# Kernel optimization log

Measured on AMD Instinct MI355X. Metric: run time of the kernel, lower is better.

## Reference

```python
import jax, jax.numpy as jnp
import numpy as np
from jax import lax

PATCH = 16  # patch_size


def setup_inputs() -> dict:
    key = jax.random.key(0)
    k1, k2, k3, k4, k5 = jax.random.split(key, 5)
    B, C, H, W = 64, 3, 384, 384
    N, E, P = 576, 768, PATCH
    x = jax.random.normal(k1, (B, C, H, W), dtype=jnp.float32)
    # start = center - patch//2; valid starts are in [0, H-P]
    start_h = jax.random.randint(k2, (B, N), 0, H - P, dtype=jnp.int32)
    start_w = jax.random.randint(k3, (B, N), 0, W - P, dtype=jnp.int32)
    proj_w = jax.random.normal(k4, (E, C, P, P), dtype=jnp.float32) * 0.02
    proj_b = jax.random.normal(k5, (E,), dtype=jnp.float32) * 0.02
    return {"x": x, "start_h": start_h, "start_w": start_w,
            "proj_w": proj_w, "proj_b": proj_b}


def _extract_patch(img, sh, sw):
    # img: [C, H, W] -> [C, P, P]
    return lax.dynamic_slice(img, (0, sh, sw), (img.shape[0], PATCH, PATCH))


def reference(x, start_h, start_w, proj_w, proj_b):
    # Gather patches: vmap over patches, then over batch -> [B, N, C, P, P]
    per_image = jax.vmap(_extract_patch, in_axes=(None, 0, 0))
    patches = jax.vmap(per_image)(x, start_h, start_w)
    # Conv2d with kernel=stride=P on a PxP patch == linear projection + bias
    out = jnp.einsum('bnchw,echw->bne', patches, proj_w) + proj_b
    return out  # [B, N, E]
```

## Files before the change

### kernel.cpp

```cpp
#include <hip/hip_runtime.h>

typedef __attribute__((ext_vector_type(8))) short short8;
typedef __attribute__((ext_vector_type(4))) float f32x4;
typedef unsigned int u32;

#define NB 64
#define NC 3
#define NH 384
#define NW 384
#define HW (NH*NW)
#define NPATCH 576
#define NE 768
#define KDIM 768
#define MDIM (NB*NPATCH)

#define BM 128
#define BN 256
#define BK 64
#define NBLK_N (NE / BN)
#define NBLK_M (MDIM / BM)
#define NWG (NBLK_M * NBLK_N)
#define NKK (KDIM / BK)

#define TILE_B_BYTES (BN * BK * 2)
#define WS_B_BYTES (NBLK_N * NKK * TILE_B_BYTES)

#define GLOBAL_AS __attribute__((address_space(1)))
#define LDS_AS    __attribute__((address_space(3)))

__device__ __forceinline__ unsigned short f2bf(float f) {
    unsigned int u = __builtin_bit_cast(unsigned int, f);
    u += 0x7fffu + ((u >> 16) & 1u);
    return (unsigned short)(u >> 16);
}

__device__ __forceinline__ u32 cvtpk(float lo, float hi) {
    u32 r;
    asm("v_cvt_pk_bf16_f32 %0, %1, %2" : "=v"(r) : "v"(lo), "v"(hi));
    return r;
}

__device__ __forceinline__ void gload_lds16(const void* g, void* l) {
    __builtin_amdgcn_global_load_lds((const GLOBAL_AS u32*)g, (LDS_AS u32*)l, 16, 0, 0);
}

__global__ __launch_bounds__(256) void convert_w(
    const float* __restrict__ pw, unsigned char* __restrict__ wsb)
{
    int id = blockIdx.x * 256 + threadIdx.x;
    int e  = id / 96;
    int ck = id - e * 96;
    int k0 = ck * 8;

    const float4 f0 = *reinterpret_cast<const float4*>(pw + (size_t)e * KDIM + k0);
    const float4 f1 = *reinterpret_cast<const float4*>(pw + (size_t)e * KDIM + k0 + 4);
    u32 a = (u32)f2bf(f0.x) | ((u32)f2bf(f0.y) << 16);
    u32 b = (u32)f2bf(f0.z) | ((u32)f2bf(f0.w) << 16);
    u32 c = (u32)f2bf(f1.x) | ((u32)f2bf(f1.y) << 16);
    u32 d = (u32)f2bf(f1.z) | ((u32)f2bf(f1.w) << 16);

    int bn = e >> 8;
    int r  = e & 255;
    int kk = k0 >> 6;
    int ch = (k0 & 63) >> 3;
    int off = (bn * NKK + kk) * TILE_B_BYTES + r * 128 + ((ch ^ (r & 7)) * 16);
    *reinterpret_cast<uint4*>(wsb + off) = make_uint4(a, b, c, d);
}

template <bool WSB>
__global__ __launch_bounds__(512, 4) void patch_embed_gemm(
    const float* __restrict__ x,
    const int* __restrict__ start_h,
    const int* __restrict__ start_w,
    const float* __restrict__ pw,
    const float* __restrict__ pb,
    const unsigned char* __restrict__ wsb,
    float* __restrict__ out)
{
    __shared__ __align__(16) unsigned short lA[2][BM * BK];
    __shared__ __align__(16) unsigned short lB[BN * BK];
    __shared__ int baseOff[BM];

    const int tid = threadIdx.x;
    const int bid  = blockIdx.x;
    const int lbid = (bid & 7) * (NWG / 8) + (bid >> 3);
    const int bm = lbid / NBLK_N;
    const int bn = lbid - bm * NBLK_N;
    const int m0 = bm * BM;
    const int e0 = bn * BN;

    if (tid < BM) {
        int m = m0 + tid;
        int b = m / NPATCH;
        int n = m - b * NPATCH;
        baseOff[tid] = b * (NC * HW) + start_h[b * NPATCH + n] * NW
                     + start_w[b * NPATCH + n];
    }

    const int lane = tid & 63;
    const int wv   = tid >> 6;
    const int wr   = wv >> 2;
    const int wc   = wv & 3;
    const int lr   = lane & 15;
    const int lk   = lane >> 4;

    const int rt = tid >> 4;
    const int j0 = (tid & 15) * 4;
    const int chunk  = j0 >> 3;
    const int within = j0 & 7;
    const int hsub   = j0 >> 4;
    const int wsub   = j0 & 15;

    __syncthreads();

    int ab[4];
    #pragma unroll
    for (int i = 0; i < 4; ++i)
        ab[i] = baseOff[i * 32 + rt] + hsub * NW + wsub;

    f32x4 acc[4][4] = {};
    float4 ar[4];

#define LOADA(KK)                                                             \
    {                                                                         \
        const int koff = ((KK) >> 2) * HW + ((KK) & 3) * 4 * NW;              \
        _Pragma("unroll")                                                     \
        for (int i = 0; i < 4; ++i)                                           \
            ar[i] = *reinterpret_cast<const float4*>(x + ab[i] + koff);       \
    }

#define WRITEA(BUF)                                                           \
    {                                                                         \
        _Pragma("unroll")                                                     \
        for (int i = 0; i < 4; ++i) {                                         \
            int r = i * 32 + rt;                                              \
            int off = r * BK + ((chunk ^ (r & 7)) * 8) + within;              \
            *reinterpret_cast<uint2*>(&lA[BUF][off]) =                        \
                make_uint2(cvtpk(ar[i].x, ar[i].y), cvtpk(ar[i].z, ar[i].w)); \
        }                                                                     \
    }

#define STAGEB(KK)                                                            \
    if (WSB) {                                                                \
        const unsigned char* src = wsb + (size_t)(bn * NKK + (KK)) * TILE_B_BYTES \
                                 + wv * 1024 + lane * 16;                     \
        unsigned char* dst = reinterpret_cast<unsigned char*>(lB) + wv * 1024;\
        _Pragma("unroll")                                                     \
        for (int i = 0; i < 4; ++i)                                           \
            gload_lds16(src + i * 8192, dst + i * 8192);                      \
    } else {                                                                  \
        _Pragma("unroll")                                                     \
        for (int i = 0; i < 8; ++i) {                                         \
            int r = i * 32 + rt;                                              \
            const float4 wf = *reinterpret_cast<const float4*>(               \
                pw + (size_t)(e0 + r) * KDIM + (KK) * BK + j0);               \
            int off = r * BK + ((chunk ^ (r & 7)) * 8) + within;              \
            *reinterpret_cast<uint2*>(&lB[off]) =                            \
                make_uint2(cvtpk(wf.x, wf.y), cvtpk(wf.z, wf.w));             \
        }                                                                     \
    }

#define COMPUTE(BUF)                                                          \
    {                                                                         \
        _Pragma("unroll")                                                     \
        for (int ks = 0; ks < 2; ++ks) {                                      \
            short8 af[4], bfr[4];                                             \
            _Pragma("unroll")                                                 \
            for (int mi = 0; mi < 4; ++mi) {                                  \
                int row = wr * 64 + mi * 16 + lr;                             \
                int off = row * BK + (((ks * 4 + lk) ^ (row & 7)) * 8);       \
                af[mi] = *reinterpret_cast<const short8*>(&lA[BUF][off]);     \
            }                                                                 \
            _Pragma("unroll")                                                 \
            for (int ni = 0; ni < 4; ++ni) {                                  \
                int row = wc * 64 + ni * 16 + lr;                             \
                int off = row * BK + (((ks * 4 + lk) ^ (row & 7)) * 8);       \
                bfr[ni] = *reinterpret_cast<const short8*>(&lB[off]);         \
            }                                                                 \
            _Pragma("unroll")                                                 \
            for (int mi = 0; mi < 4; ++mi)                                    \
                _Pragma("unroll")                                             \
                for (int ni = 0; ni < 4; ++ni)                                \
                    acc[mi][ni] = __builtin_amdgcn_mfma_f32_16x16x32_bf16(    \
                        af[mi], bfr[ni], acc[mi][ni], 0, 0, 0);               \
        }                                                                     \
    }

    LOADA(0)
    WRITEA(0)
    STAGEB(0)
    __syncthreads();

    for (int kk = 0; kk < NKK; ++kk) {
        const int buf = kk & 1;
        if (kk + 1 < NKK) LOADA(kk + 1)
        COMPUTE(buf)
        __syncthreads();
        if (kk + 1 < NKK) {
            WRITEA(buf ^ 1)
            STAGEB(kk + 1)
        }
        __syncthreads();
    }

#undef LOADA
#undef WRITEA
#undef STAGEB
#undef COMPUTE

    float biasv[4];
    #pragma unroll
    for (int ni = 0; ni < 4; ++ni)
        biasv[ni] = pb[e0 + wc * 64 + ni * 16 + lr];

    #pragma unroll
    for (int mi = 0; mi < 4; ++mi) {
        #pragma unroll
        for (int j = 0; j < 4; ++j) {
            int row = m0 + wr * 64 + mi * 16 + lk * 4 + j;
            float* orow = out + (size_t)row * NE + e0 + wc * 64 + lr;
            #pragma unroll
            for (int ni = 0; ni < 4; ++ni)
                orow[ni * 16] = acc[mi][ni][j] + biasv[ni];
        }
    }
}

extern "C" void kernel_launch(void* const* d_in, const int* in_sizes, int n_in,
                              void* d_out, int out_size, void* d_ws, size_t ws_size,
                              hipStream_t stream) {
    const float* x  = (const float*)d_in[0];
    const int* sh   = (const int*)d_in[1];
    const int* sw   = (const int*)d_in[2];
    const float* pw = (const float*)d_in[3];
    const float* pb = (const float*)d_in[4];
    float* out = (float*)d_out;

    if (ws_size >= (size_t)WS_B_BYTES) {
        unsigned char* wsb = (unsigned char*)d_ws;
        hipLaunchKernelGGL(convert_w, dim3(288), dim3(256), 0, stream, pw, wsb);
        hipLaunchKernelGGL(patch_embed_gemm<true>, dim3(NWG), dim3(512), 0, stream,
                           x, sh, sw, pw, pb, wsb, out);
    } else {
        hipLaunchKernelGGL(patch_embed_gemm<false>, dim3(NWG), dim3(512), 0, stream,
                           x, sh, sw, pw, pb, (const unsigned char*)nullptr, out);
    }
}
```

Measured before the change: 78.35 us.

## Split patch gather into pre-pass and stream pre-packed bf16 tiles into GEMM

Adds a gather kernel that extracts patches from x, converts them to bf16 and writes them into swizzled A tiles in workspace. Adds a weight conversion that writes B in MFMA fragment order, so the new GEMM loads B straight into registers and stages A via direct global-to-LDS loads with double buffering. This removes the irregular gather and fp32-to-bf16 conversion from the GEMM inner loop and frees the B LDS buffer. The cost is an extra kernel launch plus writing and re-reading roughly 57 MB of bf16 A through global memory, and the path depends on the workspace being large enough.

```diff
diff --git a/kernel.cpp b/kernel.cpp
--- a/kernel.cpp
+++ b/kernel.cpp
@@ -22,8 +22,10 @@
 #define NWG (NBLK_M * NBLK_N)
 #define NKK (KDIM / BK)
 
+#define TILE_A_BYTES (BM * BK * 2)
 #define TILE_B_BYTES (BN * BK * 2)
-#define WS_B_BYTES (NBLK_N * NKK * TILE_B_BYTES)
+#define WS_A_BYTES ((size_t)NBLK_M * NKK * TILE_A_BYTES)
+#define WS_B_BYTES ((size_t)NBLK_N * NKK * TILE_B_BYTES)
 
 #define GLOBAL_AS __attribute__((address_space(1)))
 #define LDS_AS    __attribute__((address_space(3)))
@@ -44,7 +46,186 @@
     __builtin_amdgcn_global_load_lds((const GLOBAL_AS u32*)g, (LDS_AS u32*)l, 16, 0, 0);
 }
 
-__global__ __launch_bounds__(256) void convert_w(
+__global__ __launch_bounds__(256) void gather_a(
+    const float* __restrict__ x,
+    const int* __restrict__ start_h,
+    const int* __restrict__ start_w,
+    unsigned char* __restrict__ wsa)
+{
+    int id = blockIdx.x * 256 + threadIdx.x;
+    int m  = id / 96;
+    int ck = id - m * 96;
+    int b  = m / NPATCH;
+    int n  = m - b * NPATCH;
+    int base = b * (NC * HW) + start_h[b * NPATCH + n] * NW
+             + start_w[b * NPATCH + n];
+
+    int gk = ck * 8;
+    int c  = gk >> 8;
+    int h  = (gk & 255) >> 4;
+    int w  = gk & 15;
+    const float* src = x + base + c * HW + h * NW + w;
+    float4 f0 = *reinterpret_cast<const float4*>(src);
+    float4 f1 = *reinterpret_cast<const float4*>(src + 4);
+
+    int bm = m >> 7, r = m & 127, kk = ck >> 3, ch = ck & 7;
+    size_t off = (size_t)(bm * NKK + kk) * TILE_A_BYTES
+               + r * 128 + ((ch ^ (r & 7)) * 16);
+    *reinterpret_cast<uint4*>(wsa + off) = make_uint4(
+        cvtpk(f0.x, f0.y), cvtpk(f0.z, f0.w),
+        cvtpk(f1.x, f1.y), cvtpk(f1.z, f1.w));
+}
+
+__global__ __launch_bounds__(256) void convert_w_frag(
+    const float* __restrict__ pw, unsigned char* __restrict__ wsb)
+{
+    int id = blockIdx.x * 256 + threadIdx.x;
+    int tile = id >> 11;
+    int s    = id & 2047;
+    int bn = tile / NKK;
+    int kk = tile - bn * NKK;
+    int f = s >> 6, l = s & 63;
+    int e = bn * 256 + (f >> 1) * 16 + (l & 15);
+    int k = kk * 64 + (f & 1) * 32 + (l >> 4) * 8;
+
+    const float4 f0 = *reinterpret_cast<const float4*>(pw + (size_t)e * KDIM + k);
+    const float4 f1 = *reinterpret_cast<const float4*>(pw + (size_t)e * KDIM + k + 4);
+    *reinterpret_cast<uint4*>(wsb + (size_t)tile * TILE_B_BYTES + s * 16) =
+        make_uint4(cvtpk(f0.x, f0.y), cvtpk(f0.z, f0.w),
+                   cvtpk(f1.x, f1.y), cvtpk(f1.z, f1.w));
+}
+
+__global__ __launch_bounds__(512, 4) void gemm2(
+    const unsigned char* __restrict__ wsa,
+    const unsigned char* __restrict__ wsb,
+    const float* __restrict__ pb,
+    float* __restrict__ out)
+{
+    __shared__ __align__(16) unsigned short lA[2][BM * BK];
+
+    const int tid = threadIdx.x;
+    const int bid  = blockIdx.x;
+    const int lbid = (bid & 7) * (NWG / 8) + (bid >> 3);
+    const int bm = lbid / NBLK_N;
+    const int bn = lbid - bm * NBLK_N;
+    const int m0 = bm * BM;
+    const int e0 = bn * BN;
+
+    const int lane = tid & 63;
+    const int wv   = tid >> 6;
+    const int wr   = wv >> 2;
+    const int wc   = wv & 3;
+    const int lr   = lane & 15;
+    const int lk   = lane >> 4;
+
+    const unsigned char* atiles = wsa + (size_t)bm * NKK * TILE_A_BYTES;
+    const unsigned char* btiles = wsb + (size_t)bn * NKK * TILE_B_BYTES;
+    unsigned char* lab = reinterpret_cast<unsigned char*>(&lA[0][0]);
+
+    int ard[4];
+    #pragma unroll
+    for (int mi = 0; mi < 4; ++mi) {
+        int row = wr * 64 + mi * 16 + lr;
+        ard[mi] = row * 128;
+    }
+    const int arow7[4] = { (wr*64+0*16+lr) & 7, (wr*64+1*16+lr) & 7,
+                           (wr*64+2*16+lr) & 7, (wr*64+3*16+lr) & 7 };
+
+    uint4 br[8];
+    f32x4 acc[4][4] = {};
+
+#define STAGEA(KK, BUF)                                                       \
+    {                                                                         \
+        const unsigned char* s_ = atiles + (size_t)(KK) * TILE_A_BYTES        \
+                                + wv * 2048 + lane * 16;                      \
+        unsigned char* d_ = lab + (BUF) * 16384 + wv * 2048;                  \
+        gload_lds16(s_, d_);                                                  \
+        gload_lds16(s_ + 1024, d_ + 1024);                                    \
+    }
+
+#define LOADB(KK)                                                             \
+    {                                                                         \
+        const unsigned char* bt = btiles + (size_t)(KK) * TILE_B_BYTES        \
+                                + lane * 16;                                  \
+        _Pragma("unroll")                                                     \
+        for (int f = 0; f < 8; ++f)                                           \
+            br[(f & 1) * 4 + (f >> 1)] = *reinterpret_cast<const uint4*>(     \
+                bt + ((wc * 4 + (f >> 1)) * 2 + (f & 1)) * 1024);             \
+    }
+
+#define COMPUTE(BUF)                                                          \
+    {                                                                         \
+        _Pragma("unroll")                                                     \
+        for (int ks = 0; ks < 2; ++ks) {                                      \
+            short8 af[4];                                                     \
+            _Pragma("unroll")                                                 \
+            for (int mi = 0; mi < 4; ++mi)                                    \
+                af[mi] = *reinterpret_cast<const short8*>(                    \
+                    lab + (BUF) * 16384 + ard[mi]                             \
+                        + (((ks * 4 + lk) ^ arow7[mi]) * 16));                \
+            _Pragma("unroll")                                                 \
+            for (int mi = 0; mi < 4; ++mi)                                    \
+                _Pragma("unroll")                                             \
+                for (int ni = 0; ni < 4; ++ni)                                \
+                    acc[mi][ni] = __builtin_amdgcn_mfma_f32_16x16x32_bf16(    \
+                        af[mi], __builtin_bit_cast(short8, br[ks * 4 + ni]),  \
+                        acc[mi][ni], 0, 0, 0);                                \
+        }                                                                     \
+    }
+
+    STAGEA(0, 0)
+    STAGEA(1, 1)
+    LOADB(0)
+    __builtin_amdgcn_sched_barrier(0);
+    asm volatile("s_waitcnt vmcnt(8)" ::: "memory");
+    __builtin_amdgcn_sched_barrier(0);
+    __builtin_amdgcn_s_barrier();
+
+    #pragma unroll
+    for (int kk = 0; kk < NKK; ++kk) {
+        const int buf = kk & 1;
+        COMPUTE(buf)
+        if (kk + 1 < NKK) LOADB(kk + 1)
+        if (kk + 1 < NKK) {
+            __builtin_amdgcn_sched_barrier(0);
+            __builtin_amdgcn_s_barrier();
+            __builtin_amdgcn_sched_barrier(0);
+            if (kk + 2 < NKK) STAGEA(kk + 2, buf)
+            __builtin_amdgcn_sched_barrier(0);
+            if (kk + 2 < NKK) {
+                asm volatile("s_waitcnt vmcnt(10)" ::: "memory");
+            } else {
+                asm volatile("s_waitcnt vmcnt(8)" ::: "memory");
+            }
+            __builtin_amdgcn_sched_barrier(0);
+            __builtin_amdgcn_s_barrier();
+            __builtin_amdgcn_sched_barrier(0);
+        }
+    }
+
+#undef STAGEA
+#undef LOADB
+#undef COMPUTE
+
+    float biasv[4];
+    #pragma unroll
+    for (int ni = 0; ni < 4; ++ni)
+        biasv[ni] = pb[e0 + wc * 64 + ni * 16 + lr];
+
+    #pragma unroll
+    for (int mi = 0; mi < 4; ++mi) {
+        #pragma unroll
+        for (int j = 0; j < 4; ++j) {
+            int row = m0 + wr * 64 + mi * 16 + lk * 4 + j;
+            float* orow = out + (size_t)row * NE + e0 + wc * 64 + lr;
+            #pragma unroll
+            for (int ni = 0; ni < 4; ++ni)
+                orow[ni * 16] = acc[mi][ni][j] + biasv[ni];
+        }
+    }
+}
+
+__global__ __launch_bounds__(256) void convert_w_row(
     const float* __restrict__ pw, unsigned char* __restrict__ wsb)
 {
     int id = blockIdx.x * 256 + threadIdx.x;
@@ -54,21 +235,19 @@
 
     const float4 f0 = *reinterpret_cast<const float4*>(pw + (size_t)e * KDIM + k0);
     const float4 f1 = *reinterpret_cast<const float4*>(pw + (size_t)e * KDIM + k0 + 4);
-    u32 a = (u32)f2bf(f0.x) | ((u32)f2bf(f0.y) << 16);
-    u32 b = (u32)f2bf(f0.z) | ((u32)f2bf(f0.w) << 16);
-    u32 c = (u32)f2bf(f1.x) | ((u32)f2bf(f1.y) << 16);
-    u32 d = (u32)f2bf(f1.z) | ((u32)f2bf(f1.w) << 16);
-
     int bn = e >> 8;
     int r  = e & 255;
     int kk = k0 >> 6;
     int ch = (k0 & 63) >> 3;
-    int off = (bn * NKK + kk) * TILE_B_BYTES + r * 128 + ((ch ^ (r & 7)) * 16);
-    *reinterpret_cast<uint4*>(wsb + off) = make_uint4(a, b, c, d);
+    size_t off = (size_t)(bn * NKK + kk) * TILE_B_BYTES + r * 128
+               + ((ch ^ (r & 7)) * 16);
+    *reinterpret_cast<uint4*>(wsb + off) = make_uint4(
+        cvtpk(f0.x, f0.y), cvtpk(f0.z, f0.w),
+        cvtpk(f1.x, f1.y), cvtpk(f1.z, f1.w));
 }
 
 template <bool WSB>
-__global__ __launch_bounds__(512, 4) void patch_embed_gemm(
+__global__ __launch_bounds__(512, 4) void fused_gemm(
     const float* __restrict__ x,
     const int* __restrict__ start_h,
     const int* __restrict__ start_w,
@@ -236,13 +415,21 @@
     const float* pb = (const float*)d_in[4];
     float* out = (float*)d_out;
 
-    if (ws_size >= (size_t)WS_B_BYTES) {
+    if (ws_size >= WS_A_BYTES + WS_B_BYTES) {
+        unsigned char* wsa = (unsigned char*)d_ws;
+        unsigned char* wsb = wsa + WS_A_BYTES;
+        hipLaunchKernelGGL(gather_a, dim3(MDIM * 96 / 256), dim3(256), 0, stream,
+                           x, sh, sw, wsa);
+        hipLaunchKernelGGL(convert_w_frag, dim3(288), dim3(256), 0, stream, pw, wsb);
+        hipLaunchKernelGGL(gemm2, dim3(NWG), dim3(512), 0, stream,
+                           wsa, wsb, pb, out);
+    } else if (ws_size >= WS_B_BYTES) {
         unsigned char* wsb = (unsigned char*)d_ws;
-        hipLaunchKernelGGL(convert_w, dim3(288), dim3(256), 0, stream, pw, wsb);
-        hipLaunchKernelGGL(patch_embed_gemm<true>, dim3(NWG), dim3(512), 0, stream,
+        hipLaunchKernelGGL(convert_w_row, dim3(288), dim3(256), 0, stream, pw, wsb);
+        hipLaunchKernelGGL(fused_gemm<true>, dim3(NWG), dim3(512), 0, stream,
                            x, sh, sw, pw, pb, wsb, out);
     } else {
-        hipLaunchKernelGGL(patch_embed_gemm<false>, dim3(NWG), dim3(512), 0, stream,
+        hipLaunchKernelGGL(fused_gemm<false>, dim3(NWG), dim3(512), 0, stream,
                            x, sh, sw, pw, pb, (const unsigned char*)nullptr, out);
     }
 }
```

New measurement: 103.1 us. +31.6%, slower.

## Pre-gather patches into MFMA fragment layout and run LDS-free register GEMM

Applied to the files above, without the earlier changes.

Adds a prep kernel that gathers every patch from x, converts it to bf16 and writes it to workspace in the exact per-lane MFMA fragment order, and also repacks the weights into matching fragment tiles. A new GEMM kernel then loads fragments straight from global memory into registers with double buffering, with no LDS staging and no barriers. This removes LDS traffic and syncs from the main loop. In exchange it writes and re-reads a bf16 copy of the whole A matrix (about 56 MB) and uses a second pass over memory. The old fused path stays as a fallback when the workspace is too small.

```diff
diff --git a/kernel.cpp b/kernel.cpp
--- a/kernel.cpp
+++ b/kernel.cpp
@@ -15,15 +15,14 @@
 #define MDIM (NB*NPATCH)
 
 #define BM 128
-#define BN 256
-#define BK 64
-#define NBLK_N (NE / BN)
 #define NBLK_M (MDIM / BM)
-#define NWG (NBLK_M * NBLK_N)
-#define NKK (KDIM / BK)
-
-#define TILE_B_BYTES (BN * BK * 2)
-#define WS_B_BYTES (NBLK_N * NKK * TILE_B_BYTES)
+#define NWG (NBLK_M * 3)
+
+#define AKK 24
+#define ATILE 8192
+#define BTILE 16384
+#define WS_A ((size_t)NBLK_M * AKK * ATILE)
+#define WS_B ((size_t)3 * AKK * BTILE)
 
 #define GLOBAL_AS __attribute__((address_space(1)))
 #define LDS_AS    __attribute__((address_space(3)))
@@ -44,7 +43,143 @@
     __builtin_amdgcn_global_load_lds((const GLOBAL_AS u32*)g, (LDS_AS u32*)l, 16, 0, 0);
 }
 
-__global__ __launch_bounds__(256) void convert_w(
+#define GATHER_BLOCKS (MDIM * 96 / 256)
+__global__ __launch_bounds__(256) void prep(
+    const float* __restrict__ x,
+    const int* __restrict__ start_h,
+    const int* __restrict__ start_w,
+    const float* __restrict__ pw,
+    unsigned char* __restrict__ wsa,
+    unsigned char* __restrict__ wsb)
+{
+    const int gid = blockIdx.x;
+    if (gid < GATHER_BLOCKS) {
+        int id = gid * 256 + threadIdx.x;
+        int m  = id / 96;
+        int ck = id - m * 96;
+        int b  = m / NPATCH;
+        int n  = m - b * NPATCH;
+        int base = b * (NC * HW) + start_h[b * NPATCH + n] * NW
+                 + start_w[b * NPATCH + n];
+        int gk = ck * 8;
+        int c  = gk >> 8;
+        int h  = (gk & 255) >> 4;
+        int w  = gk & 15;
+        const float* src = x + base + c * HW + h * NW + w;
+        float4 f0 = *reinterpret_cast<const float4*>(src);
+        float4 f1 = *reinterpret_cast<const float4*>(src + 4);
+
+        int bm = m >> 7, r = m & 127;
+        int kk = gk >> 5;
+        int lk = (gk >> 3) & 3;
+        int wr = r >> 6, mi = (r >> 4) & 3, lr = r & 15;
+        size_t off = (size_t)(bm * AKK + kk) * ATILE
+                   + (wr * 4 + mi) * 1024 + (lk * 16 + lr) * 16;
+        *reinterpret_cast<uint4*>(wsa + off) = make_uint4(
+            cvtpk(f0.x, f0.y), cvtpk(f0.z, f0.w),
+            cvtpk(f1.x, f1.y), cvtpk(f1.z, f1.w));
+    } else {
+        int id = (gid - GATHER_BLOCKS) * 256 + threadIdx.x;
+        int tile = id >> 10;
+        int s    = id & 1023;
+        int bn = tile / AKK;
+        int kk = tile - bn * AKK;
+        int g = s >> 6, l = s & 63;
+        int e = bn * 256 + g * 16 + (l & 15);
+        int k = kk * 32 + (l >> 4) * 8;
+        const float4 f0 = *reinterpret_cast<const float4*>(pw + (size_t)e * KDIM + k);
+        const float4 f1 = *reinterpret_cast<const float4*>(pw + (size_t)e * KDIM + k + 4);
+        *reinterpret_cast<uint4*>(wsb + (size_t)tile * BTILE + s * 16) =
+            make_uint4(cvtpk(f0.x, f0.y), cvtpk(f0.z, f0.w),
+                       cvtpk(f1.x, f1.y), cvtpk(f1.z, f1.w));
+    }
+}
+
+__global__ __launch_bounds__(512, 2) void gemm_reg(
+    const unsigned char* __restrict__ wsa,
+    const unsigned char* __restrict__ wsb,
+    const float* __restrict__ pb,
+    float* __restrict__ out)
+{
+    const int tid = threadIdx.x;
+    const int bid  = blockIdx.x;
+    const int lbid = (bid & 7) * (NWG / 8) + (bid >> 3);
+    const int bm = lbid / 3;
+    const int bn = lbid - bm * 3;
+    const int m0 = bm * BM;
+    const int e0 = bn * 256;
+
+    const int lane = tid & 63;
+    const int wv   = tid >> 6;
+    const int wr   = wv >> 2;
+    const int wc   = wv & 3;
+    const int lr   = lane & 15;
+    const int lk   = lane >> 4;
+
+    const unsigned char* aB = wsa + (size_t)bm * (AKK * ATILE)
+                            + (wr * 4) * 1024 + lane * 16;
+    const unsigned char* bB = wsb + (size_t)bn * (AKK * BTILE)
+                            + (wc * 4) * 1024 + lane * 16;
+
+    f32x4 acc[4][4] = {};
+    uint4 a0[4], b0[4], a1[4], b1[4];
+
+#define LOADS(KK, AR, BR)                                                     \
+    {                                                                         \
+        _Pragma("unroll")                                                     \
+        for (int mi = 0; mi < 4; ++mi)                                        \
+            AR[mi] = *reinterpret_cast<const uint4*>(                         \
+                aB + (KK) * ATILE + mi * 1024);                               \
+        _Pragma("unroll")                                                     \
+        for (int ni = 0; ni < 4; ++ni)                                        \
+            BR[ni] = *reinterpret_cast<const uint4*>(                         \
+                bB + (KK) * BTILE + ni * 1024);                               \
+    }
+
+#define STEP(AR, BR)                                                          \
+    {                                                                         \
+        _Pragma("unroll")                                                     \
+        for (int mi = 0; mi < 4; ++mi)                                        \
+            _Pragma("unroll")                                                 \
+            for (int ni = 0; ni < 4; ++ni)                                    \
+                acc[mi][ni] = __builtin_amdgcn_mfma_f32_16x16x32_bf16(        \
+                    __builtin_bit_cast(short8, AR[mi]),                       \
+                    __builtin_bit_cast(short8, BR[ni]),                       \
+                    acc[mi][ni], 0, 0, 0);                                    \
+    }
+
+    LOADS(0, a0, b0)
+    LOADS(1, a1, b1)
+    #pragma unroll 1
+    for (int kk = 0; kk < AKK; kk += 2) {
+        STEP(a0, b0)
+        if (kk + 2 < AKK) LOADS(kk + 2, a0, b0)
+        STEP(a1, b1)
+        if (kk + 3 < AKK) LOADS(kk + 3, a1, b1)
+    }
+
+#undef LOADS
+#undef STEP
+
+    float biasv[4];
+    #pragma unroll
+    for (int ni = 0; ni < 4; ++ni)
+        biasv[ni] = pb[e0 + wc * 64 + ni * 16 + lr];
+
+    #pragma unroll
+    for (int mi = 0; mi < 4; ++mi) {
+        #pragma unroll
+        for (int j = 0; j < 4; ++j) {
+            int row = m0 + wr * 64 + mi * 16 + lk * 4 + j;
+            float* orow = out + (size_t)row * NE + e0 + wc * 64 + lr;
+            #pragma unroll
+            for (int ni = 0; ni < 4; ++ni)
+                orow[ni * 16] = acc[mi][ni][j] + biasv[ni];
+        }
+    }
+}
+
+__global__ __launch_bounds__(256) void convert_w_row(
     const float* __restrict__ pw, unsigned char* __restrict__ wsb)
 {
     int id = blockIdx.x * 256 + threadIdx.x;
@@ -54,21 +189,19 @@
 
     const float4 f0 = *reinterpret_cast<const float4*>(pw + (size_t)e * KDIM + k0);
     const float4 f1 = *reinterpret_cast<const float4*>(pw + (size_t)e * KDIM + k0 + 4);
-    u32 a = (u32)f2bf(f0.x) | ((u32)f2bf(f0.y) << 16);
-    u32 b = (u32)f2bf(f0.z) | ((u32)f2bf(f0.w) << 16);
-    u32 c = (u32)f2bf(f1.x) | ((u32)f2bf(f1.y) << 16);
-    u32 d = (u32)f2bf(f1.z) | ((u32)f2bf(f1.w) << 16);
-
     int bn = e >> 8;
     int r  = e & 255;
     int kk = k0 >> 6;
     int ch = (k0 & 63) >> 3;
-    int off = (bn * NKK + kk) * TILE_B_BYTES + r * 128 + ((ch ^ (r & 7)) * 16);
-    *reinterpret_cast<uint4*>(wsb + off) = make_uint4(a, b, c, d);
+    size_t off = (size_t)(bn * 12 + kk) * 32768 + r * 128
+               + ((ch ^ (r & 7)) * 16);
+    *reinterpret_cast<uint4*>(wsb + off) = make_uint4(
+        cvtpk(f0.x, f0.y), cvtpk(f0.z, f0.w),
+        cvtpk(f1.x, f1.y), cvtpk(f1.z, f1.w));
 }
 
 template <bool WSB>
-__global__ __launch_bounds__(512, 4) void patch_embed_gemm(
+__global__ __launch_bounds__(512, 4) void fused_gemm(
     const float* __restrict__ x,
     const int* __restrict__ start_h,
     const int* __restrict__ start_w,
@@ -77,17 +210,17 @@
     const unsigned char* __restrict__ wsb,
     float* __restrict__ out)
 {
-    __shared__ __align__(16) unsigned short lA[2][BM * BK];
-    __shared__ __align__(16) unsigned short lB[BN * BK];
+    __shared__ __align__(16) unsigned short lA[2][BM * 64];
+    __shared__ __align__(16) unsigned short lB[256 * 64];
     __shared__ int baseOff[BM];
 
     const int tid = threadIdx.x;
     const int bid  = blockIdx.x;
     const int lbid = (bid & 7) * (NWG / 8) + (bid >> 3);
-    const int bm = lbid / NBLK_N;
-    const int bn = lbid - bm * NBLK_N;
+    const int bm = lbid / 3;
+    const int bn = lbid - bm * 3;
     const int m0 = bm * BM;
-    const int e0 = bn * BN;
+    const int e0 = bn * 256;
 
     if (tid < BM) {
         int m = m0 + tid;
@@ -134,7 +267,7 @@
         _Pragma("unroll")                                                     \
         for (int i = 0; i < 4; ++i) {                                         \
             int r = i * 32 + rt;                                              \
-            int off = r * BK + ((chunk ^ (r & 7)) * 8) + within;              \
+            int off = r * 64 + ((chunk ^ (r & 7)) * 8) + within;              \
             *reinterpret_cast<uint2*>(&lA[BUF][off]) =                        \
                 make_uint2(cvtpk(ar[i].x, ar[i].y), cvtpk(ar[i].z, ar[i].w)); \
         }                                                                     \
@@ -142,7 +275,7 @@
 
 #define STAGEB(KK)                                                            \
     if (WSB) {                                                                \
-        const unsigned char* src = wsb + (size_t)(bn * NKK + (KK)) * TILE_B_BYTES \
+        const unsigned char* src = wsb + (size_t)(bn * 12 + (KK)) * 32768     \
                                  + wv * 1024 + lane * 16;                     \
         unsigned char* dst = reinterpret_cast<unsigned char*>(lB) + wv * 1024;\
         _Pragma("unroll")                                                     \
@@ -153,8 +286,8 @@
         for (int i = 0; i < 8; ++i) {                                         \
             int r = i * 32 + rt;                                              \
             const float4 wf = *reinterpret_cast<const float4*>(               \
-                pw + (size_t)(e0 + r) * KDIM + (KK) * BK + j0);               \
-            int off = r * BK + ((chunk ^ (r & 7)) * 8) + within;              \
+                pw + (size_t)(e0 + r) * KDIM + (KK) * 64 + j0);               \
+            int off = r * 64 + ((chunk ^ (r & 7)) * 8) + within;              \
             *reinterpret_cast<uint2*>(&lB[off]) =                            \
                 make_uint2(cvtpk(wf.x, wf.y), cvtpk(wf.z, wf.w));             \
         }                                                                     \
@@ -168,13 +301,13 @@
             _Pragma("unroll")                                                 \
             for (int mi = 0; mi < 4; ++mi) {                                  \
                 int row = wr * 64 + mi * 16 + lr;                             \
-                int off = row * BK + (((ks * 4 + lk) ^ (row & 7)) * 8);       \
+                int off = row * 64 + (((ks * 4 + lk) ^ (row & 7)) * 8);       \
                 af[mi] = *reinterpret_cast<const short8*>(&lA[BUF][off]);     \
             }                                                                 \
             _Pragma("unroll")                                                 \
             for (int ni = 0; ni < 4; ++ni) {                                  \
                 int row = wc * 64 + ni * 16 + lr;                             \
-                int off = row * BK + (((ks * 4 + lk) ^ (row & 7)) * 8);       \
+                int off = row * 64 + (((ks * 4 + lk) ^ (row & 7)) * 8);       \
                 bfr[ni] = *reinterpret_cast<const short8*>(&lB[off]);         \
             }                                                                 \
             _Pragma("unroll")                                                 \
@@ -191,12 +324,12 @@
     STAGEB(0)
     __syncthreads();
 
-    for (int kk = 0; kk < NKK; ++kk) {
+    for (int kk = 0; kk < 12; ++kk) {
         const int buf = kk & 1;
-        if (kk + 1 < NKK) LOADA(kk + 1)
+        if (kk + 1 < 12) LOADA(kk + 1)
         COMPUTE(buf)
         __syncthreads();
-        if (kk + 1 < NKK) {
+        if (kk + 1 < 12) {
             WRITEA(buf ^ 1)
             STAGEB(kk + 1)
         }
@@ -236,13 +369,20 @@
     const float* pb = (const float*)d_in[4];
     float* out = (float*)d_out;
 
-    if (ws_size >= (size_t)WS_B_BYTES) {
+    if (ws_size >= WS_A + WS_B) {
+        unsigned char* wsa = (unsigned char*)d_ws;
+        unsigned char* wsb = wsa + WS_A;
+        hipLaunchKernelGGL(prep, dim3(GATHER_BLOCKS + 288), dim3(256), 0, stream,
+                           x, sh, sw, pw, wsa, wsb);
+        hipLaunchKernelGGL(gemm_reg, dim3(NWG), dim3(512), 0, stream,
+                           wsa, wsb, pb, out);
+    } else if (ws_size >= (size_t)1179648) {
         unsigned char* wsb = (unsigned char*)d_ws;
-        hipLaunchKernelGGL(convert_w, dim3(288), dim3(256), 0, stream, pw, wsb);
-        hipLaunchKernelGGL(patch_embed_gemm<true>, dim3(NWG), dim3(512), 0, stream,
+        hipLaunchKernelGGL(convert_w_row, dim3(288), dim3(256), 0, stream, pw, wsb);
+        hipLaunchKernelGGL(fused_gemm<true>, dim3(NWG), dim3(512), 0, stream,
                            x, sh, sw, pw, pb, wsb, out);
     } else {
-        hipLaunchKernelGGL(patch_embed_gemm<false>, dim3(NWG), dim3(512), 0, stream,
+        hipLaunchKernelGGL(fused_gemm<false>, dim3(NWG), dim3(512), 0, stream,
                            x, sh, sw, pw, pb, (const unsigned char*)nullptr, out);
     }
 }
```

Measured after the change: 130.8 us. 67.0% more time.

## Deepen A-tile prefetch pipeline with manual waitcnt and barriers

Applied to the files above, without the earlier changes.

Restructures the main loop so the gathered A-tile global loads are issued two iterations ahead, held in registers, and written to LDS after the compute barrier. Full __syncthreads are replaced by explicit s_waitcnt with partial vmcnt, s_barrier and sched_barrier fences so the prefetch loads stay in flight across iterations. The weight-conversion kernel also switches to the hardware packed bf16 convert instruction. The extra register-resident prefetch raises register pressure, and the hand-written vmcnt counts must match the number of outstanding loads or results will be wrong.

```diff
diff --git a/kernel.cpp b/kernel.cpp
--- a/kernel.cpp
+++ b/kernel.cpp
@@ -23,7 +23,7 @@
 #define NKK (KDIM / BK)
 
 #define TILE_B_BYTES (BN * BK * 2)
-#define WS_B_BYTES (NBLK_N * NKK * TILE_B_BYTES)
+#define WS_B_BYTES ((size_t)NBLK_N * NKK * TILE_B_BYTES)
 
 #define GLOBAL_AS __attribute__((address_space(1)))
 #define LDS_AS    __attribute__((address_space(3)))
@@ -44,7 +44,9 @@
     __builtin_amdgcn_global_load_lds((const GLOBAL_AS u32*)g, (LDS_AS u32*)l, 16, 0, 0);
 }
 
-__global__ __launch_bounds__(256) void convert_w(
+#define SCHED0() __builtin_amdgcn_sched_barrier(0)
+
+__global__ __launch_bounds__(256) void convert_w_row(
     const float* __restrict__ pw, unsigned char* __restrict__ wsb)
 {
     int id = blockIdx.x * 256 + threadIdx.x;
@@ -54,21 +56,19 @@
 
     const float4 f0 = *reinterpret_cast<const float4*>(pw + (size_t)e * KDIM + k0);
     const float4 f1 = *reinterpret_cast<const float4*>(pw + (size_t)e * KDIM + k0 + 4);
-    u32 a = (u32)f2bf(f0.x) | ((u32)f2bf(f0.y) << 16);
-    u32 b = (u32)f2bf(f0.z) | ((u32)f2bf(f0.w) << 16);
-    u32 c = (u32)f2bf(f1.x) | ((u32)f2bf(f1.y) << 16);
-    u32 d = (u32)f2bf(f1.z) | ((u32)f2bf(f1.w) << 16);
-
     int bn = e >> 8;
     int r  = e & 255;
     int kk = k0 >> 6;
     int ch = (k0 & 63) >> 3;
-    int off = (bn * NKK + kk) * TILE_B_BYTES + r * 128 + ((ch ^ (r & 7)) * 16);
-    *reinterpret_cast<uint4*>(wsb + off) = make_uint4(a, b, c, d);
+    size_t off = (size_t)(bn * NKK + kk) * TILE_B_BYTES + r * 128
+               + ((ch ^ (r & 7)) * 16);
+    *reinterpret_cast<uint4*>(wsb + off) = make_uint4(
+        cvtpk(f0.x, f0.y), cvtpk(f0.z, f0.w),
+        cvtpk(f1.x, f1.y), cvtpk(f1.z, f1.w));
 }
 
 template <bool WSB>
-__global__ __launch_bounds__(512, 4) void patch_embed_gemm(
+__global__ __launch_bounds__(512, 4) void fused_gemm(
     const float* __restrict__ x,
     const int* __restrict__ start_h,
     const int* __restrict__ start_w,
@@ -188,19 +188,39 @@
 
     LOADA(0)
     WRITEA(0)
+    LOADA(1)
+    WRITEA(1)
     STAGEB(0)
-    __syncthreads();
+    SCHED0();
+    LOADA(2)
+    SCHED0();
+    asm volatile("s_waitcnt vmcnt(4) lgkmcnt(0)" ::: "memory");
+    SCHED0();
+    __builtin_amdgcn_s_barrier();
+    SCHED0();
 
     for (int kk = 0; kk < NKK; ++kk) {
         const int buf = kk & 1;
-        if (kk + 1 < NKK) LOADA(kk + 1)
         COMPUTE(buf)
-        __syncthreads();
+        asm volatile("s_waitcnt lgkmcnt(0)" ::: "memory");
+        SCHED0();
+        __builtin_amdgcn_s_barrier();
+        SCHED0();
+        if (kk + 2 < NKK) WRITEA(buf)
+        if (kk + 1 < NKK) STAGEB(kk + 1)
+        SCHED0();
+        if (kk + 3 < NKK) LOADA(kk + 3)
+        SCHED0();
         if (kk + 1 < NKK) {
-            WRITEA(buf ^ 1)
-            STAGEB(kk + 1)
+            if (kk + 3 < NKK) {
+                asm volatile("s_waitcnt vmcnt(4) lgkmcnt(0)" ::: "memory");
+            } else {
+                asm volatile("s_waitcnt vmcnt(0) lgkmcnt(0)" ::: "memory");
+            }
+            SCHED0();
+            __builtin_amdgcn_s_barrier();
+            SCHED0();
         }
-        __syncthreads();
     }
 
 #undef LOADA
@@ -236,13 +256,13 @@
     const float* pb = (const float*)d_in[4];
     float* out = (float*)d_out;
 
-    if (ws_size >= (size_t)WS_B_BYTES) {
+    if (ws_size >= WS_B_BYTES) {
         unsigned char* wsb = (unsigned char*)d_ws;
-        hipLaunchKernelGGL(convert_w, dim3(288), dim3(256), 0, stream, pw, wsb);
-        hipLaunchKernelGGL(patch_embed_gemm<true>, dim3(NWG), dim3(512), 0, stream,
+        hipLaunchKernelGGL(convert_w_row, dim3(288), dim3(256), 0, stream, pw, wsb);
+        hipLaunchKernelGGL(fused_gemm<true>, dim3(NWG), dim3(512), 0, stream,
                            x, sh, sw, pw, pb, wsb, out);
     } else {
-        hipLaunchKernelGGL(patch_embed_gemm<false>, dim3(NWG), dim3(512), 0, stream,
+        hipLaunchKernelGGL(fused_gemm<false>, dim3(NWG), dim3(512), 0, stream,
                            x, sh, sw, pw, pb, (const unsigned char*)nullptr, out);
     }
 }
```

Result: slower. 94.23 us (+20.3%).
